# Kernel tuning notes

Hardware: AMD Instinct MI355X
Metric: run time of the kernel (lower is better)

## Reference

```python
import jax, jax.numpy as jnp
import numpy as np

B, N, K = 8, 4096, 64          # graphs, nodes per graph, clusters
E_PER = 65536                   # edges per graph (avg degree 16)
EPS = 1e-15


def gcn_conv(x, W, b, src, dst, num_nodes):
    """PyG GCNConv: add self-loops, symmetric deg^-1/2 normalization, sum-aggregate at dst."""
    h = x @ W
    loop = jnp.arange(num_nodes, dtype=src.dtype)
    s_all = jnp.concatenate([src, loop])
    d_all = jnp.concatenate([dst, loop])
    deg = jax.ops.segment_sum(jnp.ones(d_all.shape[0], dtype=h.dtype), d_all, num_segments=num_nodes)
    dis = jnp.where(deg > 0, jax.lax.rsqrt(deg), 0.0)
    msg = h[s_all] * (dis[s_all] * dis[d_all])[:, None]
    return jax.ops.segment_sum(msg, d_all, num_segments=num_nodes) + b


def setup_inputs() -> dict:
    key = jax.random.key(0)
    ks = jax.random.split(key, 12)
    F_in, H, F_out = 128, 128, 128
    x = jax.random.normal(ks[0], (B * N, F_in), dtype=jnp.float32)
    # within-graph random edges, then offset to global node ids
    local = jax.random.randint(ks[1], (2, B * E_PER), 0, N, dtype=jnp.int32)
    offs = jnp.repeat(jnp.arange(B, dtype=jnp.int32) * N, E_PER)
    edge_index = local + offs[None, :]
    batch = jnp.repeat(jnp.arange(B, dtype=jnp.int32), N)

    def lin(k, i, o):
        return (jax.random.normal(k, (i, o), dtype=jnp.float32) / np.float32(np.sqrt(i)))

    return {
        "x": x, "edge_index": edge_index, "batch": batch,
        "W1": lin(ks[2], F_in, H), "b1": jnp.zeros((H,), jnp.float32),
        "W2": lin(ks[3], H, H),    "b2": jnp.zeros((H,), jnp.float32),
        "Wa1": lin(ks[4], H, H),   "ba1": jnp.zeros((H,), jnp.float32),
        "Wa2": lin(ks[5], H, K),   "ba2": jnp.zeros((K,), jnp.float32),
        "Wo": lin(ks[6], H, F_out), "bo": jnp.zeros((F_out,), jnp.float32),
    }


def reference(x, edge_index, batch, W1, b1, W2, b2, Wa1, ba1, Wa2, ba2, Wo, bo):
    num_nodes = B * N
    src, dst = edge_index[0], edge_index[1]
    # two GCN layers (dropout inactive in eval mode)
    h = jax.nn.relu(gcn_conv(x, W1, b1, src, dst, num_nodes))
    h = gcn_conv(h, W2, b2, src, dst, num_nodes)
    # assignment MLP + softmax (module applies softmax; dense_mincut_pool re-applies it)
    s = jax.nn.softmax(jnp.tanh(h @ Wa1 + ba1) @ Wa2 + ba2, axis=-1)
    # to_dense_adj: scatter edges into [B, N, N]
    g = src // N
    adj = jnp.zeros((B, N, N), h.dtype).at[g, src % N, dst % N].add(1.0)
    # to_dense_batch: equal-size graphs -> reshape (mask all True)
    x_d = h.reshape(B, N, -1)
    s_d = jax.nn.softmax(s.reshape(B, N, K), axis=-1)  # PyG internal softmax (double softmax, faithful)
    # dense_mincut_pool
    out = jnp.einsum('bnk,bnf->bkf', s_d, x_d)              # s^T x : [B,K,F]
    As = jnp.einsum('bnm,bmk->bnk', adj, s_d)
    out_adj = jnp.einsum('bnk,bnj->bkj', s_d, As)           # s^T A s : [B,K,K]
    mincut_num = jnp.trace(out_adj, axis1=-2, axis2=-1)
    d_flat = adj.sum(-1)                                    # node degrees
    mincut_den = jnp.einsum('bnk,bn,bnk->b', s_d, d_flat, s_d)  # trace(s^T D s)
    mincut_loss = jnp.mean(-(mincut_num / mincut_den))
    ss = jnp.einsum('bnk,bnj->bkj', s_d, s_d)
    ss_n = jnp.linalg.norm(ss, axis=(-1, -2), keepdims=True)
    i_s = jnp.eye(K, dtype=ss.dtype)
    ortho_loss = jnp.mean(jnp.linalg.norm(ss / ss_n - i_s / jnp.sqrt(jnp.float32(K)), axis=(-1, -2)))
    # zero diagonal + symmetric degree normalization of pooled adj
    out_adj = out_adj * (1.0 - i_s)
    d = jnp.sqrt(out_adj.sum(-1))[:, None, :] + EPS         # [B,1,K]
    out_adj = out_adj / d / jnp.swapaxes(d, 1, 2)
    # output projection
    pooled_x = jax.nn.relu(out.reshape(-1, out.shape[-1]) @ Wo + bo)  # [B*K, F_out]
    pooled_batch = jnp.repeat(jnp.arange(B), K)
    # pooled_adj returned densely: pooled_edge_index == nonzero(pooled_adj > 0) (dynamic shape)
    return pooled_x, out_adj, pooled_batch, mincut_loss, ortho_loss
```

## Files before the change

### kernel.cpp

```cpp
#include <hip/hip_runtime.h>

#define NNODES 32768
#define NEDGES 524288
#define KCL 64
#define CPG 16

typedef _Float16 half8v __attribute__((ext_vector_type(8)));
typedef _Float16 half4v __attribute__((ext_vector_type(4)));
typedef float floatx4 __attribute__((ext_vector_type(4)));

#define WT1_OFF   0
#define WT2_OFF   16384
#define WTA1_OFF  32768
#define WTA2_OFF  49152
#define WTO_OFF   57344
#define WT_TOTAL  73728

__device__ __forceinline__ float wave_sum(float v) {
#pragma unroll
  for (int off = 32; off > 0; off >>= 1) v += __shfl_xor(v, off, 64);
  return v;
}

__global__ __launch_bounds__(256) void hist2_kernel(const int* __restrict__ src, const int* __restrict__ dst,
                                                    int* __restrict__ pIn,
                                                    const float* __restrict__ W1, const float* __restrict__ W2,
                                                    const float* __restrict__ Wa1, const float* __restrict__ Wa2,
                                                    const float* __restrict__ Wo, _Float16* __restrict__ wt16) {
  __shared__ int hIn[4096];
  const int t = threadIdx.x;
  const int g = blockIdx.x & 7;
  const int chunk = blockIdx.x >> 3;
  const int ebase = (g << 16) + (chunk << 12);
  const int nbase = g << 12;
  for (int i = t; i < 4096; i += 256) hIn[i] = 0;
  __syncthreads();
  {
    int tg = blockIdx.x * 256 + t;
#pragma unroll
    for (int i = 0; i < 3; i++) {
      int id = tg + i * 32768;
      if (id < WT_TOTAL) {
        const float* W; int base, BN;
        if (id < 16384)      { W = W1;  base = WT1_OFF;  BN = 128; }
        else if (id < 32768) { W = W2;  base = WT2_OFF;  BN = 128; }
        else if (id < 49152) { W = Wa1; base = WTA1_OFF; BN = 128; }
        else if (id < 57344) { W = Wa2; base = WTA2_OFF; BN = 64; }
        else                 { W = Wo;  base = WTO_OFF;  BN = 128; }
        int m = id - base;
        int k = m / BN, n = m % BN;
        wt16[base + n * 128 + k] = (_Float16)W[m];
      }
    }
  }
  const int4* dst4 = reinterpret_cast<const int4*>(dst + ebase);
#pragma unroll
  for (int i = 0; i < 4; ++i) {
    int4 d = dst4[i * 256 + t];
    atomicAdd(&hIn[d.x - nbase], 1);
    atomicAdd(&hIn[d.y - nbase], 1);
    atomicAdd(&hIn[d.z - nbase], 1);
    atomicAdd(&hIn[d.w - nbase], 1);
  }
  __syncthreads();
  int* dIn = pIn + ((size_t)(g * CPG + chunk) << 12);
  for (int i = t; i < 4096; i += 256) dIn[i] = hIn[i];
}

__global__ __launch_bounds__(1024) void scan2_kernel(const int* __restrict__ pIn, int* __restrict__ offs,
                                                     int* __restrict__ cbase, float* __restrict__ dis) {
  __shared__ int part[1024];
  const int t = threadIdx.x;
  const int g = blockIdx.x;
  int tot[4];
  int s = 0;
#pragma unroll
  for (int j = 0; j < 4; ++j) {
    int l = t * 4 + j;
    int cnt = 0;
#pragma unroll
    for (int c = 0; c < CPG; ++c) cnt += pIn[(((size_t)(g * CPG + c)) << 12) + l];
    tot[j] = cnt;
    s += cnt;
  }
  part[t] = s;
  __syncthreads();
  for (int off = 1; off < 1024; off <<= 1) {
    int add = (t >= off) ? part[t - off] : 0;
    __syncthreads();
    part[t] += add;
    __syncthreads();
  }
  int run = (g << 16) + ((t == 0) ? 0 : part[t - 1]);
#pragma unroll
  for (int j = 0; j < 4; ++j) {
    int l = t * 4 + j;
    int n = (g << 12) + l;
    offs[n] = run;
    dis[n] = rsqrtf((float)tot[j] + 1.0f);
    int running = run;
#pragma unroll
    for (int c = 0; c < CPG; ++c) {
      size_t idx = (((size_t)(g * CPG + c)) << 12) + l;
      cbase[idx] = running;
      running += pIn[idx];
    }
    run += tot[j];
  }
  if (g == 0 && t == 0) offs[NNODES] = NEDGES;
}

__global__ __launch_bounds__(256) void scatter2_kernel(const int* __restrict__ src, const int* __restrict__ dst,
                                                       const int* __restrict__ cbase, int* __restrict__ ssrc) {
  __shared__ int cur[4096];
  const int t = threadIdx.x;
  const int g = blockIdx.x & 7;
  const int chunk = blockIdx.x >> 3;
  const int ebase = (g << 16) + (chunk << 12);
  const int nbase = g << 12;
  const int* cb = cbase + ((size_t)(g * CPG + chunk) << 12);
  for (int i = t; i < 4096; i += 256) cur[i] = cb[i];
  __syncthreads();
  const int4* dst4 = reinterpret_cast<const int4*>(dst + ebase);
  const int4* src4 = reinterpret_cast<const int4*>(src + ebase);
#pragma unroll
  for (int i = 0; i < 4; ++i) {
    int4 d = dst4[i * 256 + t];
    int4 s = src4[i * 256 + t];
    int p0 = atomicAdd(&cur[d.x - nbase], 1); ssrc[p0] = s.x;
    int p1 = atomicAdd(&cur[d.y - nbase], 1); ssrc[p1] = s.y;
    int p2 = atomicAdd(&cur[d.z - nbase], 1); ssrc[p2] = s.z;
    int p3 = atomicAdd(&cur[d.w - nbase], 1); ssrc[p3] = s.w;
  }
}

template <int ACT, int BIAS, int SCALE, int AFP32>
__global__ __launch_bounds__(256) void mgemm_kernel(const void* __restrict__ Ain, const _Float16* __restrict__ WT16,
                                                    const float* __restrict__ bias, const float* __restrict__ rowscale,
                                                    _Float16* __restrict__ Cout) {
  __shared__ _Float16 WT[128][136];
  const int t = threadIdx.x;
  const int lane = t & 63;
  const int quad = lane >> 4, l16 = lane & 15;
  const long rowbase = (long)(blockIdx.x & 7) * 4096 + (long)(blockIdx.x >> 3) * 128 + (t >> 6) * 32;
  half8v af[2][4];
#pragma unroll
  for (int rt = 0; rt < 2; rt++)
#pragma unroll
    for (int kt = 0; kt < 4; kt++) {
      if (AFP32) {
        const float* A32 = (const float*)Ain;
        const float* p = A32 + (rowbase + rt * 16 + l16) * 128 + kt * 32 + quad * 8;
        float4 p0 = *reinterpret_cast<const float4*>(p);
        float4 p1 = *reinterpret_cast<const float4*>(p + 4);
        half8v h = {(_Float16)p0.x, (_Float16)p0.y, (_Float16)p0.z, (_Float16)p0.w,
                    (_Float16)p1.x, (_Float16)p1.y, (_Float16)p1.z, (_Float16)p1.w};
        af[rt][kt] = h;
      } else {
        const _Float16* A16 = (const _Float16*)Ain;
        af[rt][kt] = *reinterpret_cast<const half8v*>(A16 + (rowbase + rt * 16 + l16) * 128 + kt * 32 + quad * 8);
      }
    }
#pragma unroll
  for (int i = 0; i < 8; i++) {
    int idx = i * 256 + t;
    int n = idx >> 4, k8 = (idx & 15) << 3;
    *reinterpret_cast<half8v*>(&WT[n][k8]) = *reinterpret_cast<const half8v*>(&WT16[n * 128 + k8]);
  }
  __syncthreads();
  floatx4 acc[2][8];
#pragma unroll
  for (int rt = 0; rt < 2; rt++)
#pragma unroll
    for (int ct = 0; ct < 8; ct++) acc[rt][ct] = {0.f, 0.f, 0.f, 0.f};
#pragma unroll
  for (int kt = 0; kt < 4; kt++) {
    half8v bf[8];
#pragma unroll
    for (int ct = 0; ct < 8; ct++)
      bf[ct] = *reinterpret_cast<const half8v*>(&WT[ct * 16 + l16][kt * 32 + quad * 8]);
#pragma unroll
    for (int rt = 0; rt < 2; rt++)
#pragma unroll
      for (int ct = 0; ct < 8; ct++)
        acc[rt][ct] = __builtin_amdgcn_mfma_f32_16x16x32_f16(af[rt][kt], bf[ct], acc[rt][ct], 0, 0, 0);
  }
#pragma unroll
  for (int rt = 0; rt < 2; rt++) {
#pragma unroll
    for (int r = 0; r < 4; r++) {
      long row = rowbase + rt * 16 + quad * 4 + r;
      float sc = SCALE ? rowscale[row] : 1.f;
#pragma unroll
      for (int ct = 0; ct < 8; ct++) {
        float v = acc[rt][ct][r];
        if (SCALE) v *= sc;
        if (BIAS) v += bias[ct * 16 + l16];
        if (ACT == 1) v = fmaxf(v, 0.f);
        Cout[row * 128 + ct * 16 + l16] = (_Float16)v;
      }
    }
  }
}

__global__ __launch_bounds__(256) void mlp_kernel(const _Float16* __restrict__ h2, const _Float16* __restrict__ wta1,
                                                  const _Float16* __restrict__ wta2, const float* __restrict__ ba1,
                                                  const float* __restrict__ ba2, _Float16* __restrict__ sh) {
  __shared__ _Float16 WT1[128][136];
  __shared__ _Float16 Z[64][136];
  const int t = threadIdx.x;
  const int lane = t & 63;
  const int quad = lane >> 4, l16 = lane & 15;
  const int w = t >> 6;
  const long rowbase = (long)(blockIdx.x & 7) * 4096 + (long)(blockIdx.x >> 3) * 64 + w * 16;
  half8v af[4];
#pragma unroll
  for (int kt = 0; kt < 4; kt++)
    af[kt] = *reinterpret_cast<const half8v*>(h2 + (rowbase + l16) * 128 + kt * 32 + quad * 8);
#pragma unroll
  for (int i = 0; i < 8; i++) {
    int idx = i * 256 + t;
    int n = idx >> 4, k8 = (idx & 15) << 3;
    *reinterpret_cast<half8v*>(&WT1[n][k8]) = *reinterpret_cast<const half8v*>(&wta1[n * 128 + k8]);
  }
  __syncthreads();
  {
    floatx4 acc[8];
#pragma unroll
    for (int ct = 0; ct < 8; ct++) acc[ct] = {0.f, 0.f, 0.f, 0.f};
#pragma unroll
    for (int kt = 0; kt < 4; kt++) {
#pragma unroll
      for (int ct = 0; ct < 8; ct++) {
        half8v bf = *reinterpret_cast<const half8v*>(&WT1[ct * 16 + l16][kt * 32 + quad * 8]);
        acc[ct] = __builtin_amdgcn_mfma_f32_16x16x32_f16(af[kt], bf, acc[ct], 0, 0, 0);
      }
    }
#pragma unroll
    for (int r = 0; r < 4; r++) {
      int lrow = w * 16 + quad * 4 + r;
#pragma unroll
      for (int ct = 0; ct < 8; ct++) {
        float v = tanhf(acc[ct][r] + ba1[ct * 16 + l16]);
        Z[lrow][ct * 16 + l16] = (_Float16)v;
      }
    }
  }
  __syncthreads();
#pragma unroll
  for (int i = 0; i < 4; i++) {
    int idx = i * 256 + t;
    int n = idx >> 4, k8 = (idx & 15) << 3;
    *reinterpret_cast<half8v*>(&WT1[n][k8]) = *reinterpret_cast<const half8v*>(&wta2[n * 128 + k8]);
  }
  half8v af2[4];
#pragma unroll
  for (int kt = 0; kt < 4; kt++)
    af2[kt] = *reinterpret_cast<const half8v*>(&Z[w * 16 + l16][kt * 32 + quad * 8]);
  __syncthreads();
  floatx4 acc2[4];
#pragma unroll
  for (int ct = 0; ct < 4; ct++) acc2[ct] = {0.f, 0.f, 0.f, 0.f};
#pragma unroll
  for (int kt = 0; kt < 4; kt++) {
#pragma unroll
    for (int ct = 0; ct < 4; ct++) {
      half8v bf = *reinterpret_cast<const half8v*>(&WT1[ct * 16 + l16][kt * 32 + quad * 8]);
      acc2[ct] = __builtin_amdgcn_mfma_f32_16x16x32_f16(af2[kt], bf, acc2[ct], 0, 0, 0);
    }
  }
#pragma unroll
  for (int r = 0; r < 4; r++) {
    long row = rowbase + quad * 4 + r;
    float v[4];
#pragma unroll
    for (int ct = 0; ct < 4; ct++) v[ct] = acc2[ct][r] + ba2[ct * 16 + l16];
    float m = fmaxf(fmaxf(v[0], v[1]), fmaxf(v[2], v[3]));
#pragma unroll
    for (int off = 1; off <= 8; off <<= 1) m = fmaxf(m, __shfl_xor(m, off, 64));
    float se = 0.f;
#pragma unroll
    for (int ct = 0; ct < 4; ct++) { v[ct] = __expf(v[ct] - m); se += v[ct]; }
#pragma unroll
    for (int off = 1; off <= 8; off <<= 1) se += __shfl_xor(se, off, 64);
    float inv = 1.0f / se;
#pragma unroll
    for (int ct = 0; ct < 4; ct++) v[ct] *= inv;
    float m2 = fmaxf(fmaxf(v[0], v[1]), fmaxf(v[2], v[3]));
#pragma unroll
    for (int off = 1; off <= 8; off <<= 1) m2 = fmaxf(m2, __shfl_xor(m2, off, 64));
    float se2 = 0.f;
#pragma unroll
    for (int ct = 0; ct < 4; ct++) { v[ct] = __expf(v[ct] - m2); se2 += v[ct]; }
#pragma unroll
    for (int off = 1; off <= 8; off <<= 1) se2 += __shfl_xor(se2, off, 64);
    float inv2 = 1.0f / se2;
#pragma unroll
    for (int ct = 0; ct < 4; ct++) sh[row * 64 + ct * 16 + l16] = (_Float16)(v[ct] * inv2);
  }
}

__global__ __launch_bounds__(256) void aggregate_kernel(const _Float16* __restrict__ hs, const float* __restrict__ dis,
                                                        const int* __restrict__ offs, const int* __restrict__ ssrc,
                                                        const float* __restrict__ bias, _Float16* __restrict__ outh,
                                                        int relu) {
  const int lane = threadIdx.x & 63;
  const int b = blockIdx.x;
  const int node = ((b & 7) << 12) + ((b >> 3) << 2) + (threadIdx.x >> 6);
  const int q = lane >> 4;
  const int fl = (lane & 15) * 8;
  const int e0 = offs[node], e1 = offs[node + 1];
  float fa[8];
#pragma unroll
  for (int j = 0; j < 8; j++) fa[j] = 0.f;
  int e = e0;
  for (; e + 16 <= e1; e += 16) {
    int s0 = ssrc[e + q];
    int s1 = ssrc[e + 4 + q];
    int s2 = ssrc[e + 8 + q];
    int s3 = ssrc[e + 12 + q];
    half8v v0 = *reinterpret_cast<const half8v*>(hs + (size_t)s0 * 128 + fl);
    half8v v1 = *reinterpret_cast<const half8v*>(hs + (size_t)s1 * 128 + fl);
    half8v v2 = *reinterpret_cast<const half8v*>(hs + (size_t)s2 * 128 + fl);
    half8v v3 = *reinterpret_cast<const half8v*>(hs + (size_t)s3 * 128 + fl);
#pragma unroll
    for (int j = 0; j < 8; j++) fa[j] += (float)v0[j] + (float)v1[j] + (float)v2[j] + (float)v3[j];
  }
  if (e < e1) {
    int last = e1 - 1;
    int s[4]; bool m[4];
#pragma unroll
    for (int jj = 0; jj < 4; jj++) {
      int idx = e + jj * 4 + q;
      m[jj] = idx < e1;
      int sv = ssrc[idx < last ? idx : last];
      s[jj] = m[jj] ? sv : node;
    }
#pragma unroll
    for (int jj = 0; jj < 4; jj++) {
      half8v v = *reinterpret_cast<const half8v*>(hs + (size_t)s[jj] * 128 + fl);
      if (m[jj]) {
#pragma unroll
        for (int j = 0; j < 8; j++) fa[j] += (float)v[j];
      }
    }
  }
#pragma unroll
  for (int j = 0; j < 8; j++) {
    fa[j] += __shfl_xor(fa[j], 16, 64);
    fa[j] += __shfl_xor(fa[j], 32, 64);
  }
  if (q == 0) {
    float dn = dis[node];
    half8v self = *reinterpret_cast<const half8v*>(hs + (size_t)node * 128 + fl);
    float4 b0 = *reinterpret_cast<const float4*>(bias + fl);
    float4 b1 = *reinterpret_cast<const float4*>(bias + fl + 4);
    float bb[8] = {b0.x, b0.y, b0.z, b0.w, b1.x, b1.y, b1.z, b1.w};
    half8v r;
#pragma unroll
    for (int j = 0; j < 8; j++) {
      float v = fmaf(fa[j] + (float)self[j], dn, bb[j]);
      if (relu) v = fmaxf(v, 0.f);
      r[j] = (_Float16)v;
    }
    *reinterpret_cast<half8v*>(outh + (size_t)node * 128 + fl) = r;
  }
}

__global__ __launch_bounds__(256) void gather_kernel(const _Float16* __restrict__ sh, const int* __restrict__ offs,
                                                     const int* __restrict__ ssrc, _Float16* __restrict__ Gh,
                                                     float* __restrict__ dnp) {
  const int lane = threadIdx.x & 63;
  const int b = blockIdx.x;
  const int node = ((b & 7) << 12) + ((b >> 3) << 2) + (threadIdx.x >> 6);
  const int q = lane >> 3;
  const int fl = (lane & 7) * 8;
  const int e0 = offs[node], e1 = offs[node + 1];
  float fa[8];
  float sq = 0.f;
#pragma unroll
  for (int j = 0; j < 8; j++) fa[j] = 0.f;
  int e = e0;
  for (; e + 16 <= e1; e += 16) {
    int s0 = ssrc[e + q];
    int s1 = ssrc[e + 8 + q];
    half8v v0 = *reinterpret_cast<const half8v*>(sh + (size_t)s0 * 64 + fl);
    half8v v1 = *reinterpret_cast<const half8v*>(sh + (size_t)s1 * 64 + fl);
#pragma unroll
    for (int j = 0; j < 8; j++) {
      float f0 = (float)v0[j], f1 = (float)v1[j];
      fa[j] += f0 + f1;
      sq = fmaf(f0, f0, sq);
      sq = fmaf(f1, f1, sq);
    }
  }
  if (e < e1) {
    int last = e1 - 1;
    int i0 = e + q, i1 = e + 8 + q;
    bool m0 = i0 < e1, m1 = i1 < e1;
    int sv0 = ssrc[i0 < last ? i0 : last];
    int sv1 = ssrc[i1 < last ? i1 : last];
    int s0 = m0 ? sv0 : node;
    int s1 = m1 ? sv1 : node;
    half8v v0 = *reinterpret_cast<const half8v*>(sh + (size_t)s0 * 64 + fl);
    half8v v1 = *reinterpret_cast<const half8v*>(sh + (size_t)s1 * 64 + fl);
#pragma unroll
    for (int j = 0; j < 8; j++) {
      float f0 = m0 ? (float)v0[j] : 0.f;
      float f1 = m1 ? (float)v1[j] : 0.f;
      fa[j] += f0 + f1;
      sq = fmaf(f0, f0, sq);
      sq = fmaf(f1, f1, sq);
    }
  }
#pragma unroll
  for (int j = 0; j < 8; j++) {
    fa[j] += __shfl_xor(fa[j], 8, 64);
    fa[j] += __shfl_xor(fa[j], 16, 64);
    fa[j] += __shfl_xor(fa[j], 32, 64);
  }
  float den = wave_sum(sq);
  if (lane == 0) dnp[node] = den;
  if (q == 0) {
    half8v r;
#pragma unroll
    for (int j = 0; j < 8; j++) r[j] = (_Float16)fa[j];
    *reinterpret_cast<half8v*>(Gh + (size_t)node * 64 + fl) = r;
  }
}

__global__ __launch_bounds__(512) void atb_kernel(const _Float16* __restrict__ sh, const _Float16* __restrict__ Gh,
                                                  const _Float16* __restrict__ h2, float* __restrict__ pF) {
  __shared__ _Float16 XsT[64][136];
  __shared__ _Float16 YsT[256][40];
  const int t = threadIdx.x;
  const int g = blockIdx.x & 7, chunk = blockIdx.x >> 3;
  const int n0 = g * 4096 + chunk * 128;
  const int lane = t & 63;
  const int w = t >> 6;
  const int mtile = w & 3;
  const int nhalf = w >> 2;
  const int quad = lane >> 4, l16 = lane & 15;

#pragma unroll
  for (int i = 0; i < 4; i++) {
    int slot = i * 512 + t;
    int k = slot >> 4, c4 = (slot & 15) * 4;
    half4v v = *reinterpret_cast<const half4v*>(&sh[(size_t)(n0 + k) * 64 + c4]);
#pragma unroll
    for (int j = 0; j < 4; j++) XsT[c4 + j][k] = v[j];
  }

  floatx4 acc[8];
#pragma unroll
  for (int nt = 0; nt < 8; nt++) acc[nt] = {0.f, 0.f, 0.f, 0.f};

  for (int kt = 0; kt < 4; ++kt) {
    const int nb = n0 + kt * 32;
    __syncthreads();
#pragma unroll
    for (int i = 0; i < 4; i++) {
      int slot = i * 512 + t;
      int cg = slot & 15, k = (slot >> 4) & 31, ch = slot >> 9;
      int c = ch * 64 + cg * 4;
      half4v v;
      if (c < 64)       v = *reinterpret_cast<const half4v*>(&Gh[(size_t)(nb + k) * 64 + c]);
      else if (c < 128) v = *reinterpret_cast<const half4v*>(&sh[(size_t)(nb + k) * 64 + (c - 64)]);
      else              v = *reinterpret_cast<const half4v*>(&h2[(size_t)(nb + k) * 128 + (c - 128)]);
#pragma unroll
      for (int j = 0; j < 4; j++) YsT[c + j][k] = v[j];
    }
    __syncthreads();
    half8v af = *reinterpret_cast<const half8v*>(&XsT[mtile * 16 + l16][kt * 32 + quad * 8]);
#pragma unroll
    for (int nt = 0; nt < 8; nt++) {
      half8v bf = *reinterpret_cast<const half8v*>(&YsT[(nhalf * 8 + nt) * 16 + l16][quad * 8]);
      acc[nt] = __builtin_amdgcn_mfma_f32_16x16x32_f16(af, bf, acc[nt], 0, 0, 0);
    }
  }
  float* dst = pF + (size_t)blockIdx.x * 16384;
#pragma unroll
  for (int nt = 0; nt < 8; nt++) {
#pragma unroll
    for (int r = 0; r < 4; r++) {
      dst[(mtile * 16 + quad * 4 + r) * 256 + (nhalf * 8 + nt) * 16 + l16] = acc[nt][r];
    }
  }
}

__global__ __launch_bounds__(256) void merge_kernel(const float* __restrict__ pF, float* __restrict__ oadj,
                                                    float* __restrict__ ssb, _Float16* __restrict__ outp16) {
  int g = blockIdx.x & 7;
  int o4 = (blockIdx.x >> 3) * 256 + threadIdx.x;
  float sx = 0.f, sy = 0.f, sz = 0.f, sw = 0.f;
#pragma unroll
  for (int q = 0; q < 32; ++q) {
    float4 v = *reinterpret_cast<const float4*>(pF + (size_t)(q * 8 + g) * 16384 + o4 * 4);
    sx += v.x; sy += v.y; sz += v.z; sw += v.w;
  }
  int row = o4 >> 6;
  int c = (o4 & 63) * 4;
  if (c < 64) {
    float4 o = {sx, sy, sz, sw};
    *reinterpret_cast<float4*>(&oadj[g * 4096 + row * 64 + c]) = o;
  } else if (c < 128) {
    float4 o = {sx, sy, sz, sw};
    *reinterpret_cast<float4*>(&ssb[g * 4096 + row * 64 + (c - 64)]) = o;
  } else {
    half4v h = {(_Float16)sx, (_Float16)sy, (_Float16)sz, (_Float16)sw};
    *reinterpret_cast<half4v*>(&outp16[g * 8192 + row * 128 + (c - 128)]) = h;
  }
}

__global__ __launch_bounds__(256) void epilogue2_kernel(const float* __restrict__ oadj, const float* __restrict__ ssb,
                                                        const _Float16* __restrict__ outp16, const _Float16* __restrict__ wto,
                                                        const float* __restrict__ bo, const float* __restrict__ dn,
                                                        float* __restrict__ out) {
  __shared__ _Float16 outpS[64][136];
  __shared__ _Float16 WoT[128][136];
  __shared__ float red[256];
  __shared__ float rowsum[64];
  __shared__ float dw[4], w1[4], w2[4], w3[4];
  const int g = blockIdx.x, t = threadIdx.x;

#pragma unroll
  for (int i = 0; i < 8; i++) {
    int idx = i * 256 + t;
    int n = idx >> 4, k8 = (idx & 15) << 3;
    *reinterpret_cast<half8v*>(&WoT[n][k8]) = *reinterpret_cast<const half8v*>(&wto[n * 128 + k8]);
  }
#pragma unroll
  for (int i = 0; i < 4; i++) {
    int idx = i * 256 + t;
    int orow = idx >> 4, c8 = (idx & 15) * 8;
    half8v v = *reinterpret_cast<const half8v*>(&outp16[g * 8192 + orow * 128 + c8]);
    *reinterpret_cast<half8v*>(&outpS[orow][c8]) = v;
  }

  const int row = t >> 2, p = t & 3;
  float Areg[16];
  float trs_p = 0.f, ssq_p = 0.f;
#pragma unroll
  for (int c4 = 0; c4 < 4; c4++) {
    float4 a = *reinterpret_cast<const float4*>(&oadj[g * 4096 + row * 64 + p * 16 + c4 * 4]);
    Areg[c4 * 4 + 0] = a.x; Areg[c4 * 4 + 1] = a.y; Areg[c4 * 4 + 2] = a.z; Areg[c4 * 4 + 3] = a.w;
    float4 s = *reinterpret_cast<const float4*>(&ssb[g * 4096 + row * 64 + p * 16 + c4 * 4]);
    float vv[4] = {s.x, s.y, s.z, s.w};
#pragma unroll
    for (int jj = 0; jj < 4; jj++) {
      ssq_p += vv[jj] * vv[jj];
      int col = p * 16 + c4 * 4 + jj;
      if (col == row) trs_p += vv[jj];
    }
  }
  float da = 0.f;
#pragma unroll
  for (int i = 0; i < 16; i++) da += dn[g * 4096 + i * 256 + t];
  float dws = wave_sum(da);
  if ((t & 63) == 0) dw[t >> 6] = dws;

  float rs = 0.f, tra = 0.f;
#pragma unroll
  for (int c = 0; c < 16; c++) {
    int j = p * 16 + c;
    if (j == row) tra += Areg[c];
    else rs += Areg[c];
  }
  red[t] = rs;
  __syncthreads();
  if (p == 0) rowsum[row] = red[t] + red[t + 1] + red[t + 2] + red[t + 3];
  float v1 = wave_sum(tra), v2 = wave_sum(trs_p), v3 = wave_sum(ssq_p);
  if ((t & 63) == 0) { int w = t >> 6; w1[w] = v1; w2[w] = v2; w3[w] = v3; }
  __syncthreads();
  if (t == 0) {
    float TRA = w1[0] + w1[1] + w1[2] + w1[3];
    float TRS = w2[0] + w2[1] + w2[2] + w2[3];
    float SSQ = w3[0] + w3[1] + w3[2] + w3[3];
    float DEN = dw[0] + dw[1] + dw[2] + dw[3];
    atomicAdd(&out[98816], -(TRA / DEN) * 0.125f);
    float ssn = sqrtf(SSQ);
    atomicAdd(&out[98817], sqrtf(2.0f - TRS / (4.0f * ssn)) * 0.125f);
  }
  float di = sqrtf(rowsum[row]) + 1e-15f;
#pragma unroll
  for (int c = 0; c < 16; c++) {
    int j = p * 16 + c;
    float v = (j == row) ? 0.f : Areg[c];
    float dj = sqrtf(rowsum[j]) + 1e-15f;
    out[65536 + g * 4096 + row * 64 + j] = v / (di * dj);
  }
  if (t < 64) out[98304 + g * 64 + t] = (float)g;

  const int lane = t & 63;
  const int quad = lane >> 4, l16 = lane & 15;
  const int w = t >> 6;
  floatx4 acc[8];
#pragma unroll
  for (int ct = 0; ct < 8; ct++) acc[ct] = {0.f, 0.f, 0.f, 0.f};
#pragma unroll
  for (int kt = 0; kt < 4; kt++) {
    half8v af = *reinterpret_cast<const half8v*>(&outpS[w * 16 + l16][kt * 32 + quad * 8]);
#pragma unroll
    for (int ct = 0; ct < 8; ct++) {
      half8v bf = *reinterpret_cast<const half8v*>(&WoT[ct * 16 + l16][kt * 32 + quad * 8]);
      acc[ct] = __builtin_amdgcn_mfma_f32_16x16x32_f16(af, bf, acc[ct], 0, 0, 0);
    }
  }
#pragma unroll
  for (int r = 0; r < 4; r++) {
    int orow = w * 16 + quad * 4 + r;
#pragma unroll
    for (int ct = 0; ct < 8; ct++) {
      int col = ct * 16 + l16;
      float v = fmaxf(acc[ct][r] + bo[col], 0.f);
      out[(g * 64 + orow) * 128 + col] = v;
    }
  }
}

extern "C" void kernel_launch(void* const* d_in, const int* in_sizes, int n_in,
                              void* d_out, int out_size, void* d_ws, size_t ws_size,
                              hipStream_t stream) {
  const float* x   = (const float*)d_in[0];
  const int*   ei  = (const int*)d_in[1];
  const float* W1  = (const float*)d_in[3];
  const float* b1  = (const float*)d_in[4];
  const float* W2  = (const float*)d_in[5];
  const float* b2  = (const float*)d_in[6];
  const float* Wa1 = (const float*)d_in[7];
  const float* ba1 = (const float*)d_in[8];
  const float* Wa2 = (const float*)d_in[9];
  const float* ba2 = (const float*)d_in[10];
  const float* Wo  = (const float*)d_in[11];
  const float* bo  = (const float*)d_in[12];
  const int* src = ei;
  const int* dst = ei + NEDGES;
  float* out = (float*)d_out;

  char* ws = (char*)d_ws;
  size_t o = 0;
  auto alloc = [&](size_t bytes) -> void* {
    void* p = ws + o;
    o += (bytes + 255) & ~(size_t)255;
    return p;
  };
  _Float16* h16A = (_Float16*)alloc((size_t)NNODES * 128 * 2);
  _Float16* h16B = (_Float16*)alloc((size_t)NNODES * 128 * 2);
  _Float16* h16C = (_Float16*)alloc((size_t)NNODES * 128 * 2);
  _Float16* sh   = (_Float16*)alloc((size_t)NNODES * 64 * 2);
  _Float16* Gh   = (_Float16*)alloc((size_t)NNODES * 64 * 2);
  float* pF    = (float*)alloc((size_t)256 * 16384 * 4);
  float* dis   = (float*)alloc((size_t)NNODES * 4);
  int* offs    = (int*)alloc((size_t)(NNODES + 1) * 4);
  int* ssrc    = (int*)alloc((size_t)NEDGES * 4);
  int* pIn     = (int*)alloc((size_t)8 * CPG * 4096 * 4);
  int* cbase   = (int*)alloc((size_t)8 * CPG * 4096 * 4);
  float* dn    = (float*)alloc((size_t)NNODES * 4);
  float* oadj  = (float*)alloc(8 * 4096 * 4);
  float* ssb   = (float*)alloc(8 * 4096 * 4);
  _Float16* outp16 = (_Float16*)alloc(8 * 8192 * 2);
  _Float16* wt16   = (_Float16*)alloc((size_t)WT_TOTAL * 2);

  hipMemsetAsync(out + 98816, 0, 2 * sizeof(float), stream);

  hist2_kernel<<<8 * CPG, 256, 0, stream>>>(src, dst, pIn, W1, W2, Wa1, Wa2, Wo, wt16);
  scan2_kernel<<<8, 1024, 0, stream>>>(pIn, offs, cbase, dis);
  scatter2_kernel<<<8 * CPG, 256, 0, stream>>>(src, dst, cbase, ssrc);

  mgemm_kernel<0, 0, 1, 1><<<NNODES / 128, 256, 0, stream>>>(x, wt16 + WT1_OFF, nullptr, dis, h16A);
  aggregate_kernel<<<NNODES / 4, 256, 0, stream>>>(h16A, dis, offs, ssrc, b1, h16B, 1);
  mgemm_kernel<0, 0, 1, 0><<<NNODES / 128, 256, 0, stream>>>(h16B, wt16 + WT2_OFF, nullptr, dis, h16A);
  aggregate_kernel<<<NNODES / 4, 256, 0, stream>>>(h16A, dis, offs, ssrc, b2, h16C, 0);

  mlp_kernel<<<NNODES / 64, 256, 0, stream>>>(h16C, wt16 + WTA1_OFF, wt16 + WTA2_OFF, ba1, ba2, sh);

  gather_kernel<<<NNODES / 4, 256, 0, stream>>>(sh, offs, ssrc, Gh, dn);
  atb_kernel<<<256, 512, 0, stream>>>(sh, Gh, h16C, pF);
  merge_kernel<<<128, 256, 0, stream>>>(pF, oadj, ssb, outp16);
  epilogue2_kernel<<<8, 256, 0, stream>>>(oadj, ssb, outp16, wt16 + WTO_OFF, bo, dn, out);
}
```

Before: 196.8 us.

## Fuse first GEMM into histogram launch, reuse atomic ranks in scatter, halve atb blocks

The histogram kernel now also runs the first feature GEMM in extra blocks, which convert W1 to half precision themselves. It records each edge's intra-chunk rank from the shared-memory atomic. The scatter kernel uses those stored ranks instead of redoing the atomics, and it applies the deferred dis row scaling to the GEMM output. The atb reduction gives each block 256 nodes instead of 128, so there are half as many partial tiles for merge to sum. The aim is fewer launches and less atomic and partial-buffer traffic, at the cost of an extra rank buffer and a rounding-order change from scaling after fp16 storage.

```diff
diff --git a/kernel.cpp b/kernel.cpp
--- a/kernel.cpp
+++ b/kernel.cpp
@@ -8,6 +8,7 @@
 typedef _Float16 half8v __attribute__((ext_vector_type(8)));
 typedef _Float16 half4v __attribute__((ext_vector_type(4)));
 typedef float floatx4 __attribute__((ext_vector_type(4)));
+typedef unsigned short ushort4v __attribute__((ext_vector_type(4)));
 
 #define WT1_OFF   0
 #define WT2_OFF   16384
@@ -22,49 +23,111 @@
   return v;
 }
 
-__global__ __launch_bounds__(256) void hist2_kernel(const int* __restrict__ src, const int* __restrict__ dst,
-                                                    int* __restrict__ pIn,
-                                                    const float* __restrict__ W1, const float* __restrict__ W2,
-                                                    const float* __restrict__ Wa1, const float* __restrict__ Wa2,
-                                                    const float* __restrict__ Wo, _Float16* __restrict__ wt16) {
-  __shared__ int hIn[4096];
+__global__ __launch_bounds__(256) void histmm_kernel(const int* __restrict__ src, const int* __restrict__ dst,
+                                                     int* __restrict__ pIn, unsigned short* __restrict__ rank16,
+                                                     const float* __restrict__ W1, const float* __restrict__ W2,
+                                                     const float* __restrict__ Wa1, const float* __restrict__ Wa2,
+                                                     const float* __restrict__ Wo, _Float16* __restrict__ wt16,
+                                                     const float* __restrict__ x, _Float16* __restrict__ h16A) {
+  __shared__ _Float16 WT[128][136];
   const int t = threadIdx.x;
-  const int g = blockIdx.x & 7;
-  const int chunk = blockIdx.x >> 3;
-  const int ebase = (g << 16) + (chunk << 12);
-  const int nbase = g << 12;
-  for (int i = t; i < 4096; i += 256) hIn[i] = 0;
-  __syncthreads();
-  {
-    int tg = blockIdx.x * 256 + t;
-#pragma unroll
-    for (int i = 0; i < 3; i++) {
-      int id = tg + i * 32768;
-      if (id < WT_TOTAL) {
-        const float* W; int base, BN;
-        if (id < 16384)      { W = W1;  base = WT1_OFF;  BN = 128; }
-        else if (id < 32768) { W = W2;  base = WT2_OFF;  BN = 128; }
-        else if (id < 49152) { W = Wa1; base = WTA1_OFF; BN = 128; }
-        else if (id < 57344) { W = Wa2; base = WTA2_OFF; BN = 64; }
-        else                 { W = Wo;  base = WTO_OFF;  BN = 128; }
-        int m = id - base;
-        int k = m / BN, n = m % BN;
-        wt16[base + n * 128 + k] = (_Float16)W[m];
-      }
-    }
-  }
-  const int4* dst4 = reinterpret_cast<const int4*>(dst + ebase);
-#pragma unroll
-  for (int i = 0; i < 4; ++i) {
-    int4 d = dst4[i * 256 + t];
-    atomicAdd(&hIn[d.x - nbase], 1);
-    atomicAdd(&hIn[d.y - nbase], 1);
-    atomicAdd(&hIn[d.z - nbase], 1);
-    atomicAdd(&hIn[d.w - nbase], 1);
-  }
-  __syncthreads();
-  int* dIn = pIn + ((size_t)(g * CPG + chunk) << 12);
-  for (int i = t; i < 4096; i += 256) dIn[i] = hIn[i];
+  if (blockIdx.x < 128) {
+    int* hIn = (int*)&WT[0][0];
+    const int g = blockIdx.x & 7;
+    const int chunk = blockIdx.x >> 3;
+    const int ebase = (g << 16) + (chunk << 12);
+    const int nbase = g << 12;
+    for (int i = t; i < 4096; i += 256) hIn[i] = 0;
+    __syncthreads();
+    {
+      int tg = blockIdx.x * 256 + t;
+#pragma unroll
+      for (int i = 0; i < 3; i++) {
+        int id = tg + i * 32768;
+        if (id < WT_TOTAL) {
+          const float* W; int base, BN;
+          if (id < 16384)      { W = W1;  base = WT1_OFF;  BN = 128; }
+          else if (id < 32768) { W = W2;  base = WT2_OFF;  BN = 128; }
+          else if (id < 49152) { W = Wa1; base = WTA1_OFF; BN = 128; }
+          else if (id < 57344) { W = Wa2; base = WTA2_OFF; BN = 64; }
+          else                 { W = Wo;  base = WTO_OFF;  BN = 128; }
+          int m = id - base;
+          int k = m / BN, n = m % BN;
+          wt16[base + n * 128 + k] = (_Float16)W[m];
+        }
+      }
+    }
+    const int4* dst4 = reinterpret_cast<const int4*>(dst + ebase);
+    ushort4v* rank4 = reinterpret_cast<ushort4v*>(rank16) + ((size_t)ebase >> 2);
+#pragma unroll
+    for (int i = 0; i < 4; ++i) {
+      int4 d = dst4[i * 256 + t];
+      ushort4v r;
+      r[0] = (unsigned short)atomicAdd(&hIn[d.x - nbase], 1);
+      r[1] = (unsigned short)atomicAdd(&hIn[d.y - nbase], 1);
+      r[2] = (unsigned short)atomicAdd(&hIn[d.z - nbase], 1);
+      r[3] = (unsigned short)atomicAdd(&hIn[d.w - nbase], 1);
+      rank4[i * 256 + t] = r;
+    }
+    __syncthreads();
+    int* dIn = pIn + ((size_t)(g * CPG + chunk) << 12);
+    for (int i = t; i < 4096; i += 256) dIn[i] = hIn[i];
+  } else {
+    const int bid = blockIdx.x - 128;
+    const int lane = t & 63;
+    const int quad = lane >> 4, l16 = lane & 15;
+    const long rowbase = (long)(bid & 7) * 4096 + (long)(bid >> 3) * 128 + (t >> 6) * 32;
+    half8v af[2][4];
+#pragma unroll
+    for (int rt = 0; rt < 2; rt++)
+#pragma unroll
+      for (int kt = 0; kt < 4; kt++) {
+        const float* p = x + (rowbase + rt * 16 + l16) * 128 + kt * 32 + quad * 8;
+        float4 p0 = *reinterpret_cast<const float4*>(p);
+        float4 p1 = *reinterpret_cast<const float4*>(p + 4);
+        half8v h = {(_Float16)p0.x, (_Float16)p0.y, (_Float16)p0.z, (_Float16)p0.w,
+                    (_Float16)p1.x, (_Float16)p1.y, (_Float16)p1.z, (_Float16)p1.w};
+        af[rt][kt] = h;
+      }
+#pragma unroll
+    for (int i = 0; i < 16; i++) {
+      int idx = i * 256 + t;
+      int k = idx >> 5, n4 = (idx & 31) * 4;
+      float4 w = *reinterpret_cast<const float4*>(W1 + k * 128 + n4);
+      WT[n4 + 0][k] = (_Float16)w.x;
+      WT[n4 + 1][k] = (_Float16)w.y;
+      WT[n4 + 2][k] = (_Float16)w.z;
+      WT[n4 + 3][k] = (_Float16)w.w;
+    }
+    __syncthreads();
+    floatx4 acc[2][8];
+#pragma unroll
+    for (int rt = 0; rt < 2; rt++)
+#pragma unroll
+      for (int ct = 0; ct < 8; ct++) acc[rt][ct] = {0.f, 0.f, 0.f, 0.f};
+#pragma unroll
+    for (int kt = 0; kt < 4; kt++) {
+      half8v bf[8];
+#pragma unroll
+      for (int ct = 0; ct < 8; ct++)
+        bf[ct] = *reinterpret_cast<const half8v*>(&WT[ct * 16 + l16][kt * 32 + quad * 8]);
+#pragma unroll
+      for (int rt = 0; rt < 2; rt++)
+#pragma unroll
+        for (int ct = 0; ct < 8; ct++)
+          acc[rt][ct] = __builtin_amdgcn_mfma_f32_16x16x32_f16(af[rt][kt], bf[ct], acc[rt][ct], 0, 0, 0);
+    }
+#pragma unroll
+    for (int rt = 0; rt < 2; rt++) {
+#pragma unroll
+      for (int r = 0; r < 4; r++) {
+        long row = rowbase + rt * 16 + quad * 4 + r;
+#pragma unroll
+        for (int ct = 0; ct < 8; ct++)
+          h16A[row * 128 + ct * 16 + l16] = (_Float16)acc[rt][ct][r];
+      }
+    }
+  }
 }
 
 __global__ __launch_bounds__(1024) void scan2_kernel(const int* __restrict__ pIn, int* __restrict__ offs,
@@ -110,27 +173,43 @@
   if (g == 0 && t == 0) offs[NNODES] = NEDGES;
 }
 
-__global__ __launch_bounds__(256) void scatter2_kernel(const int* __restrict__ src, const int* __restrict__ dst,
-                                                       const int* __restrict__ cbase, int* __restrict__ ssrc) {
-  __shared__ int cur[4096];
+__global__ __launch_bounds__(256) void scatter3_kernel(const int* __restrict__ src, const int* __restrict__ dst,
+                                                       const unsigned short* __restrict__ rank16,
+                                                       const int* __restrict__ cbase, int* __restrict__ ssrc,
+                                                       const float* __restrict__ dis, _Float16* __restrict__ h16A) {
   const int t = threadIdx.x;
   const int g = blockIdx.x & 7;
   const int chunk = blockIdx.x >> 3;
   const int ebase = (g << 16) + (chunk << 12);
   const int nbase = g << 12;
   const int* cb = cbase + ((size_t)(g * CPG + chunk) << 12);
-  for (int i = t; i < 4096; i += 256) cur[i] = cb[i];
-  __syncthreads();
   const int4* dst4 = reinterpret_cast<const int4*>(dst + ebase);
   const int4* src4 = reinterpret_cast<const int4*>(src + ebase);
+  const ushort4v* rank4 = reinterpret_cast<const ushort4v*>(rank16) + ((size_t)ebase >> 2);
 #pragma unroll
   for (int i = 0; i < 4; ++i) {
     int4 d = dst4[i * 256 + t];
     int4 s = src4[i * 256 + t];
-    int p0 = atomicAdd(&cur[d.x - nbase], 1); ssrc[p0] = s.x;
-    int p1 = atomicAdd(&cur[d.y - nbase], 1); ssrc[p1] = s.y;
-    int p2 = atomicAdd(&cur[d.z - nbase], 1); ssrc[p2] = s.z;
-    int p3 = atomicAdd(&cur[d.w - nbase], 1); ssrc[p3] = s.w;
+    ushort4v r = rank4[i * 256 + t];
+    ssrc[cb[d.x - nbase] + r[0]] = s.x;
+    ssrc[cb[d.y - nbase] + r[1]] = s.y;
+    ssrc[cb[d.z - nbase] + r[2]] = s.z;
+    ssrc[cb[d.w - nbase] + r[3]] = s.w;
+  }
+  const int lane = t & 63;
+  const int w = t >> 6;
+#pragma unroll
+  for (int i = 0; i < 4; ++i) {
+    int row = nbase + (chunk << 8) + (i * 4 + w) * 16 + (lane >> 2);
+    int c8 = (lane & 3) * 32 + 0;
+    float sc = dis[row];
+#pragma unroll
+    for (int seg = 0; seg < 4; ++seg) {
+      half8v v = *reinterpret_cast<half8v*>(&h16A[(size_t)row * 128 + c8 + seg * 8]);
+#pragma unroll
+      for (int j = 0; j < 8; j++) v[j] = (_Float16)((float)v[j] * sc);
+      *reinterpret_cast<half8v*>(&h16A[(size_t)row * 128 + c8 + seg * 8]) = v;
+    }
   }
 }
 
@@ -435,47 +514,50 @@
   __shared__ _Float16 YsT[256][40];
   const int t = threadIdx.x;
   const int g = blockIdx.x & 7, chunk = blockIdx.x >> 3;
-  const int n0 = g * 4096 + chunk * 128;
+  const int n0 = g * 4096 + chunk * 256;
   const int lane = t & 63;
   const int w = t >> 6;
   const int mtile = w & 3;
   const int nhalf = w >> 2;
   const int quad = lane >> 4, l16 = lane & 15;
 
-#pragma unroll
-  for (int i = 0; i < 4; i++) {
-    int slot = i * 512 + t;
-    int k = slot >> 4, c4 = (slot & 15) * 4;
-    half4v v = *reinterpret_cast<const half4v*>(&sh[(size_t)(n0 + k) * 64 + c4]);
-#pragma unroll
-    for (int j = 0; j < 4; j++) XsT[c4 + j][k] = v[j];
-  }
-
   floatx4 acc[8];
 #pragma unroll
   for (int nt = 0; nt < 8; nt++) acc[nt] = {0.f, 0.f, 0.f, 0.f};
 
-  for (int kt = 0; kt < 4; ++kt) {
-    const int nb = n0 + kt * 32;
+  for (int half = 0; half < 2; ++half) {
+    const int hb = n0 + half * 128;
     __syncthreads();
 #pragma unroll
     for (int i = 0; i < 4; i++) {
       int slot = i * 512 + t;
-      int cg = slot & 15, k = (slot >> 4) & 31, ch = slot >> 9;
-      int c = ch * 64 + cg * 4;
-      half4v v;
-      if (c < 64)       v = *reinterpret_cast<const half4v*>(&Gh[(size_t)(nb + k) * 64 + c]);
-      else if (c < 128) v = *reinterpret_cast<const half4v*>(&sh[(size_t)(nb + k) * 64 + (c - 64)]);
-      else              v = *reinterpret_cast<const half4v*>(&h2[(size_t)(nb + k) * 128 + (c - 128)]);
-#pragma unroll
-      for (int j = 0; j < 4; j++) YsT[c + j][k] = v[j];
-    }
-    __syncthreads();
-    half8v af = *reinterpret_cast<const half8v*>(&XsT[mtile * 16 + l16][kt * 32 + quad * 8]);
-#pragma unroll
-    for (int nt = 0; nt < 8; nt++) {
-      half8v bf = *reinterpret_cast<const half8v*>(&YsT[(nhalf * 8 + nt) * 16 + l16][quad * 8]);
-      acc[nt] = __builtin_amdgcn_mfma_f32_16x16x32_f16(af, bf, acc[nt], 0, 0, 0);
+      int k = slot >> 4, c4 = (slot & 15) * 4;
+      half4v v = *reinterpret_cast<const half4v*>(&sh[(size_t)(hb + k) * 64 + c4]);
+#pragma unroll
+      for (int j = 0; j < 4; j++) XsT[c4 + j][k] = v[j];
+    }
+    for (int kt = 0; kt < 4; ++kt) {
+      const int nb = hb + kt * 32;
+      __syncthreads();
+#pragma unroll
+      for (int i = 0; i < 4; i++) {
+        int slot = i * 512 + t;
+        int cg = slot & 15, k = (slot >> 4) & 31, ch = slot >> 9;
+        int c = ch * 64 + cg * 4;
+        half4v v;
+        if (c < 64)       v = *reinterpret_cast<const half4v*>(&Gh[(size_t)(nb + k) * 64 + c]);
+        else if (c < 128) v = *reinterpret_cast<const half4v*>(&sh[(size_t)(nb + k) * 64 + (c - 64)]);
+        else              v = *reinterpret_cast<const half4v*>(&h2[(size_t)(nb + k) * 128 + (c - 128)]);
+#pragma unroll
+        for (int j = 0; j < 4; j++) YsT[c + j][k] = v[j];
+      }
+      __syncthreads();
+      half8v af = *reinterpret_cast<const half8v*>(&XsT[mtile * 16 + l16][kt * 32 + quad * 8]);
+#pragma unroll
+      for (int nt = 0; nt < 8; nt++) {
+        half8v bf = *reinterpret_cast<const half8v*>(&YsT[(nhalf * 8 + nt) * 16 + l16][quad * 8]);
+        acc[nt] = __builtin_amdgcn_mfma_f32_16x16x32_f16(af, bf, acc[nt], 0, 0, 0);
+      }
     }
   }
   float* dst = pF + (size_t)blockIdx.x * 16384;
@@ -494,7 +576,7 @@
   int o4 = (blockIdx.x >> 3) * 256 + threadIdx.x;
   float sx = 0.f, sy = 0.f, sz = 0.f, sw = 0.f;
 #pragma unroll
-  for (int q = 0; q < 32; ++q) {
+  for (int q = 0; q < 16; ++q) {
     float4 v = *reinterpret_cast<const float4*>(pF + (size_t)(q * 8 + g) * 16384 + o4 * 4);
     sx += v.x; sy += v.y; sz += v.z; sw += v.w;
   }
@@ -649,10 +731,11 @@
   _Float16* h16C = (_Float16*)alloc((size_t)NNODES * 128 * 2);
   _Float16* sh   = (_Float16*)alloc((size_t)NNODES * 64 * 2);
   _Float16* Gh   = (_Float16*)alloc((size_t)NNODES * 64 * 2);
-  float* pF    = (float*)alloc((size_t)256 * 16384 * 4);
+  float* pF    = (float*)alloc((size_t)128 * 16384 * 4);
   float* dis   = (float*)alloc((size_t)NNODES * 4);
   int* offs    = (int*)alloc((size_t)(NNODES + 1) * 4);
   int* ssrc    = (int*)alloc((size_t)NEDGES * 4);
+  unsigned short* rank16 = (unsigned short*)alloc((size_t)NEDGES * 2);
   int* pIn     = (int*)alloc((size_t)8 * CPG * 4096 * 4);
   int* cbase   = (int*)alloc((size_t)8 * CPG * 4096 * 4);
   float* dn    = (float*)alloc((size_t)NNODES * 4);
@@ -663,11 +746,10 @@
 
   hipMemsetAsync(out + 98816, 0, 2 * sizeof(float), stream);
 
-  hist2_kernel<<<8 * CPG, 256, 0, stream>>>(src, dst, pIn, W1, W2, Wa1, Wa2, Wo, wt16);
+  histmm_kernel<<<384, 256, 0, stream>>>(src, dst, pIn, rank16, W1, W2, Wa1, Wa2, Wo, wt16, x, h16A);
   scan2_kernel<<<8, 1024, 0, stream>>>(pIn, offs, cbase, dis);
-  scatter2_kernel<<<8 * CPG, 256, 0, stream>>>(src, dst, cbase, ssrc);
-
-  mgemm_kernel<0, 0, 1, 1><<<NNODES / 128, 256, 0, stream>>>(x, wt16 + WT1_OFF, nullptr, dis, h16A);
+  scatter3_kernel<<<128, 256, 0, stream>>>(src, dst, rank16, cbase, ssrc, dis, h16A);
+
   aggregate_kernel<<<NNODES / 4, 256, 0, stream>>>(h16A, dis, offs, ssrc, b1, h16B, 1);
   mgemm_kernel<0, 0, 1, 0><<<NNODES / 128, 256, 0, stream>>>(h16B, wt16 + WT2_OFF, nullptr, dis, h16A);
   aggregate_kernel<<<NNODES / 4, 256, 0, stream>>>(h16A, dis, offs, ssrc, b2, h16C, 0);
@@ -675,7 +757,7 @@
   mlp_kernel<<<NNODES / 64, 256, 0, stream>>>(h16C, wt16 + WTA1_OFF, wt16 + WTA2_OFF, ba1, ba2, sh);
 
   gather_kernel<<<NNODES / 4, 256, 0, stream>>>(sh, offs, ssrc, Gh, dn);
-  atb_kernel<<<256, 512, 0, stream>>>(sh, Gh, h16C, pF);
+  atb_kernel<<<128, 512, 0, stream>>>(sh, Gh, h16C, pF);
   merge_kernel<<<128, 256, 0, stream>>>(pF, oadj, ssb, outp16);
   epilogue2_kernel<<<8, 256, 0, stream>>>(oadj, ssb, outp16, wt16 + WTO_OFF, bo, dn, out);
 }
```

New measurement: 203.7 us. 1.04x slower.
